# Performance work log

Measured on AMD Instinct MI355X. Metric: run time of the kernel, lower is better.

The kernel has to match this reference:

```python
import jax, jax.numpy as jnp
import numpy as np

B, N, F_DIM = 64, 4096, 64
K_SLOTS, D, N_ITERS = 8, 64, 3
EPS = 1e-8
LN_EPS = 1e-5  # torch LayerNorm default


def layernorm(x, g, b):
    mu = jnp.mean(x, axis=-1, keepdims=True)
    var = jnp.mean(jnp.square(x - mu), axis=-1, keepdims=True)
    return (x - mu) * jax.lax.rsqrt(var + LN_EPS) * g + b


def gru_cell(x, h, w_ih, w_hh, b_ih, b_hh):
    # torch.nn.GRUCell semantics; weights are [3D, D] with gate order r, z, n
    gi = x @ w_ih.T + b_ih
    gh = h @ w_hh.T + b_hh
    i_r, i_z, i_n = jnp.split(gi, 3, axis=-1)
    h_r, h_z, h_n = jnp.split(gh, 3, axis=-1)
    r = jax.nn.sigmoid(i_r + h_r)
    z = jax.nn.sigmoid(i_z + h_z)
    n = jnp.tanh(i_n + r * h_n)
    return (1.0 - z) * n + z * h


def setup_inputs() -> dict:
    key = jax.random.key(0)
    ks = jax.random.split(key, 16)
    f32 = jnp.float32
    s = 0.05  # small init scale for weights
    return {
        "inputs": jax.random.normal(ks[0], (B, N, F_DIM), f32),
        "slots_noise": jax.random.normal(ks[1], (B, K_SLOTS, D), f32),
        "slots_mu": jax.random.normal(ks[2], (1, 1, D), f32) * s,
        "slots_log_sigma": jax.random.normal(ks[3], (1, 1, D), f32) * s,
        "Wq": jax.random.normal(ks[4], (D, D), f32) * s,
        "Wk": jax.random.normal(ks[5], (D, F_DIM), f32) * s,
        "Wv": jax.random.normal(ks[6], (D, F_DIM), f32) * s,
        "gru_w_ih": jax.random.normal(ks[7], (3 * D, D), f32) * s,
        "gru_w_hh": jax.random.normal(ks[8], (3 * D, D), f32) * s,
        "gru_b_ih": jnp.zeros((3 * D,), f32),
        "gru_b_hh": jnp.zeros((3 * D,), f32),
        "mlp_w1": jax.random.normal(ks[9], (2 * D, D), f32) * s,
        "mlp_b1": jnp.zeros((2 * D,), f32),
        "mlp_w2": jax.random.normal(ks[10], (D, 2 * D), f32) * s,
        "mlp_b2": jnp.zeros((D,), f32),
        "ln_in_g": jnp.ones((F_DIM,), f32), "ln_in_b": jnp.zeros((F_DIM,), f32),
        "ln_slots_g": jnp.ones((D,), f32), "ln_slots_b": jnp.zeros((D,), f32),
        "ln_mlp_g": jnp.ones((D,), f32), "ln_mlp_b": jnp.zeros((D,), f32),
    }


def reference(inputs, slots_noise, slots_mu, slots_log_sigma, Wq, Wk, Wv,
              gru_w_ih, gru_w_hh, gru_b_ih, gru_b_hh,
              mlp_w1, mlp_b1, mlp_w2, mlp_b2,
              ln_in_g, ln_in_b, ln_slots_g, ln_slots_b, ln_mlp_g, ln_mlp_b):
    x = layernorm(inputs, ln_in_g, ln_in_b)          # [B, N, F]
    k = jnp.einsum('bnf,df->bnd', x, Wk)             # [B, N, D]
    v = jnp.einsum('bnf,df->bnd', x, Wv)             # [B, N, D]

    slots = slots_mu + jnp.exp(slots_log_sigma) * slots_noise  # [B, K, D]
    scale = D ** -0.5

    for _ in range(N_ITERS):
        slots_prev = slots
        s_n = layernorm(slots, ln_slots_g, ln_slots_b)
        q = jnp.einsum('bkd,ed->bke', s_n, Wq)                  # [B, K, D]
        attn_logits = jnp.einsum('bnd,bkd->bnk', k, q) * scale  # [B, N, K]
        attn = jax.nn.softmax(attn_logits, axis=-1) + EPS       # softmax over slots
        attn = attn / jnp.sum(attn, axis=1, keepdims=True)      # renormalize over N
        updates = jnp.einsum('bnk,bnd->bkd', attn, v)           # [B, K, D]
        slots = gru_cell(updates.reshape(-1, D), slots_prev.reshape(-1, D),
                         gru_w_ih, gru_w_hh, gru_b_ih, gru_b_hh).reshape(B, K_SLOTS, D)
        h = layernorm(slots, ln_mlp_g, ln_mlp_b)
        h = jax.nn.relu(h @ mlp_w1.T + mlp_b1) @ mlp_w2.T + mlp_b2
        slots = slots + h
    return slots
```

## Files before the change

kernel.cpp:

```cpp
#include <hip/hip_runtime.h>
#include <math.h>

#define NN 4096
#define LN_EPS 1e-5f
#define EPS 1e-8f

typedef unsigned short ushortT;
typedef unsigned int uintT;
typedef __attribute__((ext_vector_type(8))) short short8;
typedef __attribute__((ext_vector_type(4))) float f32x4;
typedef __attribute__((ext_vector_type(4))) unsigned short us4;

#define OFF_KT    0L
#define OFF_V     16777216L
#define OFF_QT    33554432L
#define OFF_ACC   33587200L
#define OFF_COL   33619968L
#define OFF_SLOTS 33620480L
#define OFF_WIHT  33653248L
#define OFF_WHHT  33665536L
#define OFF_W1T   33677824L
#define OFF_W2T   33686016L
#define OFF_WQT   33694208L
#define OFF_WKV   33698304L
#define OFF_CNT   33702400L

__device__ __forceinline__ float wredsum(float v) {
#pragma unroll
  for (int off = 32; off > 0; off >>= 1) v += __shfl_xor(v, off);
  return v;
}

__device__ __forceinline__ ushortT f2bf(float f) {
  uintT b = __float_as_uint(f);
  b += 0x7fff + ((b >> 16) & 1);
  return (ushortT)(b >> 16);
}

__global__ __launch_bounds__(256) void k_prep(
    const float* __restrict__ w_ih, const float* __restrict__ w_hh,
    const float* __restrict__ w1, const float* __restrict__ w2,
    const float* __restrict__ Wq,
    const float* __restrict__ Wk, const float* __restrict__ Wv,
    float* __restrict__ wihT, float* __restrict__ whhT,
    float* __restrict__ w1T, float* __restrict__ w2T, float* __restrict__ wqT,
    ushortT* __restrict__ wpack, uintT* __restrict__ cnt)
{
  int idx = blockIdx.x * 256 + threadIdx.x;
  if (idx < 12288) {
    int j = idx >> 6, f = idx & 63;
    wihT[f * 192 + j] = w_ih[idx];
  } else if (idx < 24576) {
    int i = idx - 12288; int j = i >> 6, f = i & 63;
    whhT[f * 192 + j] = w_hh[i];
  } else if (idx < 32768) {
    int i = idx - 24576; int j = i >> 6, f = i & 63;
    w1T[f * 128 + j] = w1[i];
  } else if (idx < 40960) {
    int i = idx - 32768; int d = i >> 7, j = i & 127;
    w2T[j * 64 + d] = w2[i];
  } else if (idx < 45056) {
    int i = idx - 40960; int e = i >> 6, d = i & 63;
    wqT[d * 64 + e] = Wq[i];
  } else if (idx < 53248) {
    int i = idx - 45056;
    int j = i & 7, l = (i >> 3) & 63, t2 = i >> 9;
    int ct = t2 >> 1, kb = t2 & 1;
    int kf = kb * 32 + ((l >> 4) << 3) + j;
    int col = (ct << 4) | (l & 15);
    float val = (col < 64) ? Wk[col * 64 + kf] : Wv[(col - 64) * 64 + kf];
    wpack[i] = f2bf(val);
  } else if (idx < 53312) {
    cnt[idx - 53248] = 0u;
  }
}

__global__ __launch_bounds__(256) void k_ln_init(
    const float* __restrict__ inp, const ushortT* __restrict__ wpack,
    const float* __restrict__ g, const float* __restrict__ bbv,
    ushortT* __restrict__ ktF, ushortT* __restrict__ vF,
    const float* __restrict__ noise, const float* __restrict__ smu,
    const float* __restrict__ slsig, const float* __restrict__ wqT,
    const float* __restrict__ g_sl, const float* __restrict__ b_sl,
    float* __restrict__ slots, ushortT* __restrict__ qF,
    float* __restrict__ acc, float* __restrict__ colsum)
{
  __shared__ __align__(16) ushortT xnF[4096];
  __shared__ __align__(16) ushortT kS[4096];
  const int tid = threadIdx.x;
  const int lane = tid & 63;
  const int wave = tid >> 6;

  if (blockIdx.x >= 4096) {
    const int bi = blockIdx.x - 4096;
    const int row = bi * 4 + wave;
    const int b = row >> 3, ks = row & 7;
    float* S2 = (float*)&xnF[0];

    float s0 = fmaf(expf(slsig[lane]), noise[row * 64 + lane], smu[lane]);
    slots[row * 64 + lane] = s0;
    acc[row * 64 + lane] = 0.f;
    if (lane == 0) colsum[row] = 0.f;

    float mu = wredsum(s0) * (1.f / 64.f);
    float dx = s0 - mu;
    float var = wredsum(dx * dx) * (1.f / 64.f);
    float sn = dx * rsqrtf(var + LN_EPS) * g_sl[lane] + b_sl[lane];
    S2[(wave << 6) + lane] = sn;
    __syncthreads();
    float qe = 0.f;
#pragma unroll 16
    for (int d = 0; d < 64; ++d) qe = fmaf(S2[(wave << 6) + d], wqT[d * 64 + lane], qe);
    const int kb = lane >> 5, lrow = (lane & 31) >> 3, j = lane & 7;
    qF[((((b * 2 + kb) << 6) + (lrow << 4) + ks) << 3) + j] = f2bf(qe * 0.125f);
    qF[((((b * 2 + kb) << 6) + (lrow << 4) + 8 + ks) << 3) + j] = 0;
    return;
  }

  const int l15 = lane & 15, q = lane >> 4;
  const int tile = blockIdx.x;
  const int b = tile >> 6;
  const int c = tile & 63;
  const int n0 = c << 6;
  const float* rowbase = inp + (((long)b * NN + n0) << 6);
  const float4 g4 = *(const float4*)&g[l15 << 2];
  const float4 b4 = *(const float4*)&bbv[l15 << 2];

#pragma unroll
  for (int i = 0; i < 4; ++i) {
    const int row = (wave << 4) + (i << 2) + q;
    float4 x = *(const float4*)&rowbase[(row << 6) + (l15 << 2)];
    float s = x.x + x.y + x.z + x.w;
    s += __shfl_xor(s, 1); s += __shfl_xor(s, 2);
    s += __shfl_xor(s, 4); s += __shfl_xor(s, 8);
    const float mu = s * (1.f / 64.f);
    float4 dx = {x.x - mu, x.y - mu, x.z - mu, x.w - mu};
    float ss = dx.x * dx.x + dx.y * dx.y + dx.z * dx.z + dx.w * dx.w;
    ss += __shfl_xor(ss, 1); ss += __shfl_xor(ss, 2);
    ss += __shfl_xor(ss, 4); ss += __shfl_xor(ss, 8);
    const float rs = rsqrtf(ss * (1.f / 64.f) + LN_EPS);
    us4 p = {f2bf(dx.x * rs * g4.x + b4.x), f2bf(dx.y * rs * g4.y + b4.y),
             f2bf(dx.z * rs * g4.z + b4.z), f2bf(dx.w * rs * g4.w + b4.w)};
    *(us4*)&xnF[((((wave << 1) + (l15 >> 3)) << 6) + (((l15 & 7) >> 1) << 4)
                 + (row & 15)) * 8 + ((l15 & 1) << 2)] = p;
  }

  short8 bfrag[2][2];
#pragma unroll
  for (int nt = 0; nt < 2; ++nt)
#pragma unroll
    for (int kb = 0; kb < 2; ++kb)
      bfrag[nt][kb] = *(const short8*)&wpack[((((2 * wave + nt) << 1) | kb) * 64 + lane) << 3];

  __syncthreads();

  f32x4 acc4[4][2];
#pragma unroll
  for (int mt = 0; mt < 4; ++mt)
#pragma unroll
    for (int nt = 0; nt < 2; ++nt) acc4[mt][nt] = (f32x4){0.f, 0.f, 0.f, 0.f};

#pragma unroll
  for (int mt = 0; mt < 4; ++mt) {
    short8 a0 = *(const short8*)&xnF[((mt * 2 + 0) * 64 + lane) << 3];
    short8 a1 = *(const short8*)&xnF[((mt * 2 + 1) * 64 + lane) << 3];
#pragma unroll
    for (int nt = 0; nt < 2; ++nt) {
      acc4[mt][nt] = __builtin_amdgcn_mfma_f32_16x16x32_bf16(a0, bfrag[nt][0], acc4[mt][nt], 0, 0, 0);
      acc4[mt][nt] = __builtin_amdgcn_mfma_f32_16x16x32_bf16(a1, bfrag[nt][1], acc4[mt][nt], 0, 0, 0);
    }
  }

  if (wave < 2) {
#pragma unroll
    for (int mt = 0; mt < 4; ++mt)
#pragma unroll
      for (int nt = 0; nt < 2; ++nt) {
        const int base = (((mt * 2 + wave) << 6) + ((2 * nt + (l15 >> 3)) << 4) + (q << 2));
#pragma unroll
        for (int r = 0; r < 4; ++r)
          kS[((base + r) << 3) + (l15 & 7)] = f2bf(acc4[mt][nt][r]);
      }
  } else {
    ushortT* vbase = vF + ((long)(b * 64 + c) << 12);
#pragma unroll
    for (int mt = 0; mt < 4; ++mt)
#pragma unroll
      for (int nt = 0; nt < 2; ++nt) {
        const int ntg = 2 * (wave - 2) + nt;
        us4 p = {f2bf(acc4[mt][nt][0]), f2bf(acc4[mt][nt][1]),
                 f2bf(acc4[mt][nt][2]), f2bf(acc4[mt][nt][3])};
        *(us4*)&vbase[(((((ntg << 1) + (mt >> 1)) << 6)
                        + (((mt & 1) * 2 + (q >> 1)) << 4) + l15) << 3)
                      + ((q & 1) << 2)] = p;
      }
  }
  __syncthreads();

  ushortT* kdst = ktF + ((long)(b * 64 + c) << 12);
  short8 v0 = *(const short8*)&kS[tid << 4];
  short8 v1 = *(const short8*)&kS[(tid << 4) + 8];
  *(short8*)&kdst[tid << 4] = v0;
  *(short8*)&kdst[(tid << 4) + 8] = v1;
}

__global__ __launch_bounds__(256) void k_attn(
    const ushortT* __restrict__ ktF, const ushortT* __restrict__ vF,
    ushortT* __restrict__ qF,
    float* __restrict__ acc, float* __restrict__ colsum,
    uintT* __restrict__ cnt, float* __restrict__ slots,
    const float* __restrict__ wihT, const float* __restrict__ whhT,
    const float* __restrict__ w1T, const float* __restrict__ w2T,
    const float* __restrict__ wqT,
    const float* __restrict__ b_ih, const float* __restrict__ b_hh,
    const float* __restrict__ mb1, const float* __restrict__ mb2,
    const float* __restrict__ g_ml, const float* __restrict__ b_ml,
    const float* __restrict__ g_sl, const float* __restrict__ b_sl,
    float* __restrict__ dout)
{
  __shared__ __align__(16) ushortT attnF[4][1024];
  __shared__ float accLds[4][8][64];
  __shared__ float colLds[4][8];
  __shared__ int lastFlag;
  const int tid = threadIdx.x;
  const int lane = tid & 63;
  const int wave = tid >> 6;
  const int l15 = lane & 15, q = lane >> 4;
  const int b = blockIdx.x >> 4;
  const int chunk = ((blockIdx.x & 15) << 2) | wave;

  const ushortT* kbF = ktF + ((long)(b * 64 + chunk) << 12);
  const ushortT* vbF = vF + ((long)(b * 64 + chunk) << 12);

  short8 kA[4][2];
#pragma unroll
  for (int mt = 0; mt < 4; ++mt)
#pragma unroll
    for (int kb = 0; kb < 2; ++kb)
      kA[mt][kb] = *(const short8*)&kbF[((mt * 2 + kb) * 64 + lane) << 3];
  short8 qB[2];
#pragma unroll
  for (int kb = 0; kb < 2; ++kb)
    qB[kb] = *(const short8*)&qF[(((b * 2 + kb) << 6) + lane) << 3];

  f32x4 accL[4];
#pragma unroll
  for (int mt = 0; mt < 4; ++mt) {
    accL[mt] = (f32x4){0.f, 0.f, 0.f, 0.f};
    accL[mt] = __builtin_amdgcn_mfma_f32_16x16x32_bf16(kA[mt][0], qB[0], accL[mt], 0, 0, 0);
    accL[mt] = __builtin_amdgcn_mfma_f32_16x16x32_bf16(kA[mt][1], qB[1], accL[mt], 0, 0, 0);
  }

  short8 vB[4][2];
#pragma unroll
  for (int nt = 0; nt < 4; ++nt)
#pragma unroll
    for (int ks = 0; ks < 2; ++ks)
      vB[nt][ks] = *(const short8*)&vbF[((nt * 2 + ks) * 64 + lane) << 3];

  float csum = 0.f;
#pragma unroll
  for (int mt = 0; mt < 4; ++mt) {
    float av[4];
#pragma unroll
    for (int r = 0; r < 4; ++r) {
      float lv = accL[mt][r];
      float mx = lv;
      mx = fmaxf(mx, __shfl_xor(mx, 1));
      mx = fmaxf(mx, __shfl_xor(mx, 2));
      mx = fmaxf(mx, __shfl_xor(mx, 4));
      float ev = __expf(lv - mx);
      float sv = ev;
      sv += __shfl_xor(sv, 1); sv += __shfl_xor(sv, 2); sv += __shfl_xor(sv, 4);
      float a = ev * (1.f / sv) + EPS;
      av[r] = a;
      csum += a;
    }
    us4 p = {f2bf(av[0]), f2bf(av[1]), f2bf(av[2]), f2bf(av[3])};
    *(us4*)&attnF[wave][((((mt >> 1) << 6) + (((mt & 1) * 2 + (q >> 1)) << 4)
                          + l15) << 3) + ((q & 1) << 2)] = p;
  }
  csum += __shfl_xor(csum, 16);
  csum += __shfl_xor(csum, 32);

  short8 pA0 = *(const short8*)&attnF[wave][(0 * 64 + lane) << 3];
  short8 pA1 = *(const short8*)&attnF[wave][(1 * 64 + lane) << 3];

  f32x4 accP[4];
#pragma unroll
  for (int nt = 0; nt < 4; ++nt) {
    accP[nt] = (f32x4){0.f, 0.f, 0.f, 0.f};
    accP[nt] = __builtin_amdgcn_mfma_f32_16x16x32_bf16(pA0, vB[nt][0], accP[nt], 0, 0, 0);
    accP[nt] = __builtin_amdgcn_mfma_f32_16x16x32_bf16(pA1, vB[nt][1], accP[nt], 0, 0, 0);
  }

  if (q < 2) {
#pragma unroll
    for (int nt = 0; nt < 4; ++nt)
#pragma unroll
      for (int r = 0; r < 4; ++r)
        accLds[wave][q * 4 + r][nt * 16 + l15] = accP[nt][r];
  }
  if (q == 0 && l15 < 8) colLds[wave][l15] = csum;
  __syncthreads();

#pragma unroll
  for (int r = 0; r < 2; ++r) {
    const int o = tid + r * 256;
    const int kk = o >> 6, d = o & 63;
    float s = accLds[0][kk][d] + accLds[1][kk][d] + accLds[2][kk][d] + accLds[3][kk][d];
    atomicAdd(&acc[(b * 8 + kk) * 64 + d], s);
  }
  if (tid < 8) {
    float s = colLds[0][tid] + colLds[1][tid] + colLds[2][tid] + colLds[3][tid];
    atomicAdd(&colsum[b * 8 + tid], s);
  }

  __syncthreads();
  if (tid == 0) lastFlag = (atomicAdd(&cnt[b], 1u) == 15u);
  __syncthreads();
  if (!lastFlag) return;

  const int ks0 = wave, ks1 = wave + 4;
  const int row0 = b * 8 + ks0, row1 = b * 8 + ks1;

  float csv0 = 0.f, csv1 = 0.f;
  if (lane == 0) {
    csv0 = atomicAdd(&colsum[row0], 0.f);
    csv1 = atomicAdd(&colsum[row1], 0.f);
  }
  csv0 = __shfl(csv0, 0); csv1 = __shfl(csv1, 0);
  const float u0 = atomicAdd(&acc[row0 * 64 + lane], 0.f) / csv0;
  const float u1 = atomicAdd(&acc[row1 * 64 + lane], 0.f) / csv1;
  const float h0 = slots[row0 * 64 + lane];
  const float h1 = slots[row1 * 64 + lane];

  float* S = (float*)&attnF[wave][0];
  S[lane] = u0; S[64 + lane] = u1; S[128 + lane] = h0; S[192 + lane] = h1;

  float gir0 = b_ih[lane], giz0 = b_ih[64 + lane], gin0 = b_ih[128 + lane];
  float ghr0 = b_hh[lane], ghz0 = b_hh[64 + lane], ghn0 = b_hh[128 + lane];
  float gir1 = gir0, giz1 = giz0, gin1 = gin0;
  float ghr1 = ghr0, ghz1 = ghz0, ghn1 = ghn0;
#pragma unroll 4
  for (int f = 0; f < 64; ++f) {
    const float wr = wihT[f * 192 + lane], wz = wihT[f * 192 + 64 + lane],
                wn = wihT[f * 192 + 128 + lane];
    const float vr = whhT[f * 192 + lane], vz = whhT[f * 192 + 64 + lane],
                vn = whhT[f * 192 + 128 + lane];
    const float a0 = S[f], a1 = S[64 + f], c0 = S[128 + f], c1 = S[192 + f];
    gir0 = fmaf(a0, wr, gir0); gir1 = fmaf(a1, wr, gir1);
    giz0 = fmaf(a0, wz, giz0); giz1 = fmaf(a1, wz, giz1);
    gin0 = fmaf(a0, wn, gin0); gin1 = fmaf(a1, wn, gin1);
    ghr0 = fmaf(c0, vr, ghr0); ghr1 = fmaf(c1, vr, ghr1);
    ghz0 = fmaf(c0, vz, ghz0); ghz1 = fmaf(c1, vz, ghz1);
    ghn0 = fmaf(c0, vn, ghn0); ghn1 = fmaf(c1, vn, ghn1);
  }
  const float r0 = 1.f / (1.f + expf(-(gir0 + ghr0)));
  const float z0 = 1.f / (1.f + expf(-(giz0 + ghz0)));
  const float n0 = tanhf(fmaf(r0, ghn0, gin0));
  const float hn0 = (1.f - z0) * n0 + z0 * h0;
  const float r1 = 1.f / (1.f + expf(-(gir1 + ghr1)));
  const float z1 = 1.f / (1.f + expf(-(giz1 + ghz1)));
  const float n1 = tanhf(fmaf(r1, ghn1, gin1));
  const float hn1 = (1.f - z1) * n1 + z1 * h1;

  float mu0 = wredsum(hn0) * (1.f / 64.f);
  float dx0 = hn0 - mu0;
  float va0 = wredsum(dx0 * dx0) * (1.f / 64.f);
  const float ln0 = dx0 * rsqrtf(va0 + LN_EPS) * g_ml[lane] + b_ml[lane];
  float mu1 = wredsum(hn1) * (1.f / 64.f);
  float dx1 = hn1 - mu1;
  float va1 = wredsum(dx1 * dx1) * (1.f / 64.f);
  const float ln1 = dx1 * rsqrtf(va1 + LN_EPS) * g_ml[lane] + b_ml[lane];
  S[256 + lane] = ln0; S[320 + lane] = ln1;

  float h1a0 = mb1[lane], h1b0 = mb1[64 + lane];
  float h1a1 = h1a0, h1b1 = h1b0;
#pragma unroll 4
  for (int f = 0; f < 64; ++f) {
    const float wa = w1T[f * 128 + lane], wb = w1T[f * 128 + 64 + lane];
    const float l0 = S[256 + f], l1 = S[320 + f];
    h1a0 = fmaf(l0, wa, h1a0); h1a1 = fmaf(l1, wa, h1a1);
    h1b0 = fmaf(l0, wb, h1b0); h1b1 = fmaf(l1, wb, h1b1);
  }
  h1a0 = fmaxf(h1a0, 0.f); h1b0 = fmaxf(h1b0, 0.f);
  h1a1 = fmaxf(h1a1, 0.f); h1b1 = fmaxf(h1b1, 0.f);
  S[lane] = h1a0; S[64 + lane] = h1b0;
  S[128 + lane] = h1a1; S[192 + lane] = h1b1;

  float o0 = mb2[lane], o1 = mb2[lane];
#pragma unroll 4
  for (int j = 0; j < 128; ++j) {
    const float w2v = w2T[j * 64 + lane];
    o0 = fmaf(S[j], w2v, o0);
    o1 = fmaf(S[128 + j], w2v, o1);
  }
  const float sn0 = hn0 + o0;
  const float sn1 = hn1 + o1;
  slots[row0 * 64 + lane] = sn0;
  slots[row1 * 64 + lane] = sn1;
  if (dout) {
    dout[row0 * 64 + lane] = sn0;
    dout[row1 * 64 + lane] = sn1;
  }

  float m20 = wredsum(sn0) * (1.f / 64.f);
  float d20 = sn0 - m20;
  float v20 = wredsum(d20 * d20) * (1.f / 64.f);
  const float sq0 = d20 * rsqrtf(v20 + LN_EPS) * g_sl[lane] + b_sl[lane];
  float m21 = wredsum(sn1) * (1.f / 64.f);
  float d21 = sn1 - m21;
  float v21 = wredsum(d21 * d21) * (1.f / 64.f);
  const float sq1 = d21 * rsqrtf(v21 + LN_EPS) * g_sl[lane] + b_sl[lane];
  S[256 + lane] = sq0; S[320 + lane] = sq1;
  float qe0 = 0.f, qe1 = 0.f;
#pragma unroll 8
  for (int d = 0; d < 64; ++d) {
    const float wq = wqT[d * 64 + lane];
    qe0 = fmaf(S[256 + d], wq, qe0);
    qe1 = fmaf(S[320 + d], wq, qe1);
  }
  const int kb = lane >> 5, lrow = (lane & 31) >> 3, jj = lane & 7;
  qF[((((b * 2 + kb) << 6) + (lrow << 4) + ks0) << 3) + jj] = f2bf(qe0 * 0.125f);
  qF[((((b * 2 + kb) << 6) + (lrow << 4) + ks1) << 3) + jj] = f2bf(qe1 * 0.125f);

  acc[row0 * 64 + lane] = 0.f;
  acc[row1 * 64 + lane] = 0.f;
  if (lane == 0) { colsum[row0] = 0.f; colsum[row1] = 0.f; }
  if (tid == 0) cnt[b] = 0u;
}

extern "C" void kernel_launch(void* const* d_in, const int* in_sizes, int n_in,
                              void* d_out, int out_size, void* d_ws, size_t ws_size,
                              hipStream_t stream) {
  const float* inp   = (const float*)d_in[0];
  const float* noise = (const float*)d_in[1];
  const float* smu   = (const float*)d_in[2];
  const float* slsig = (const float*)d_in[3];
  const float* Wq    = (const float*)d_in[4];
  const float* Wk    = (const float*)d_in[5];
  const float* Wv    = (const float*)d_in[6];
  const float* w_ih  = (const float*)d_in[7];
  const float* w_hh  = (const float*)d_in[8];
  const float* b_ih  = (const float*)d_in[9];
  const float* b_hh  = (const float*)d_in[10];
  const float* w1    = (const float*)d_in[11];
  const float* b1    = (const float*)d_in[12];
  const float* w2    = (const float*)d_in[13];
  const float* b2    = (const float*)d_in[14];
  const float* g_in  = (const float*)d_in[15];
  const float* bi_in = (const float*)d_in[16];
  const float* g_sl  = (const float*)d_in[17];
  const float* bi_sl = (const float*)d_in[18];
  const float* g_ml  = (const float*)d_in[19];
  const float* bi_ml = (const float*)d_in[20];

  float* ws      = (float*)d_ws;
  ushortT* ktF   = (ushortT*)(ws + OFF_KT);
  ushortT* vF    = (ushortT*)(ws + OFF_V);
  ushortT* qF    = (ushortT*)(ws + OFF_QT);
  float* ac      = ws + OFF_ACC;
  float* cs      = ws + OFF_COL;
  float* sl      = ws + OFF_SLOTS;
  float* wihT    = ws + OFF_WIHT;
  float* whhT    = ws + OFF_WHHT;
  float* w1T     = ws + OFF_W1T;
  float* w2T     = ws + OFF_W2T;
  float* wqT     = ws + OFF_WQT;
  ushortT* wpk   = (ushortT*)(ws + OFF_WKV);
  uintT* cnt     = (uintT*)(ws + OFF_CNT);

  k_prep<<<209, 256, 0, stream>>>(w_ih, w_hh, w1, w2, Wq, Wk, Wv,
                                  wihT, whhT, w1T, w2T, wqT, wpk, cnt);
  k_ln_init<<<4224, 256, 0, stream>>>(inp, wpk, g_in, bi_in, ktF, vF,
                                      noise, smu, slsig, wqT, g_sl, bi_sl,
                                      sl, qF, ac, cs);
  for (int it = 0; it < 3; ++it) {
    k_attn<<<1024, 256, 0, stream>>>(ktF, vF, qF, ac, cs, cnt, sl,
                                     wihT, whhT, w1T, w2T, wqT,
                                     b_ih, b_hh, b1, b2, g_ml, bi_ml, g_sl, bi_sl,
                                     it == 2 ? (float*)d_out : nullptr);
  }
}
```

Before: 259.8 us.

## Fold Wk into query and Wv after aggregation to store only normalized inputs

Instead of materializing K and V (two bf16 tensors) from the layernormed inputs, the kernel stores only the normalized input x once and folds Wk into the query (q·Wk) and applies Wv after the attention-weighted sum of x. This halves the large per-iteration global reads of K/V and removes the K/V MFMA projection from the init kernel. It adds small per-slot matvecs in the attention kernel and an LDS transpose of the x fragments to build the V-side operand. That transpose carries bank-conflict and register costs, and bf16 rounding now happens at different points.

```diff
diff --git a/kernel.cpp b/kernel.cpp
--- a/kernel.cpp
+++ b/kernel.cpp
@@ -11,8 +11,7 @@
 typedef __attribute__((ext_vector_type(4))) float f32x4;
 typedef __attribute__((ext_vector_type(4))) unsigned short us4;
 
-#define OFF_KT    0L
-#define OFF_V     16777216L
+#define OFF_XN    0L
 #define OFF_QT    33554432L
 #define OFF_ACC   33587200L
 #define OFF_COL   33619968L
@@ -22,7 +21,7 @@
 #define OFF_W1T   33677824L
 #define OFF_W2T   33686016L
 #define OFF_WQT   33694208L
-#define OFF_WKV   33698304L
+#define OFF_WVT   33698304L
 #define OFF_CNT   33702400L
 
 __device__ __forceinline__ float wredsum(float v) {
@@ -40,11 +39,10 @@
 __global__ __launch_bounds__(256) void k_prep(
     const float* __restrict__ w_ih, const float* __restrict__ w_hh,
     const float* __restrict__ w1, const float* __restrict__ w2,
-    const float* __restrict__ Wq,
-    const float* __restrict__ Wk, const float* __restrict__ Wv,
+    const float* __restrict__ Wq, const float* __restrict__ Wv,
     float* __restrict__ wihT, float* __restrict__ whhT,
     float* __restrict__ w1T, float* __restrict__ w2T, float* __restrict__ wqT,
-    ushortT* __restrict__ wpack, uintT* __restrict__ cnt)
+    float* __restrict__ wvT, uintT* __restrict__ cnt)
 {
   int idx = blockIdx.x * 256 + threadIdx.x;
   if (idx < 12288) {
@@ -62,31 +60,26 @@
   } else if (idx < 45056) {
     int i = idx - 40960; int e = i >> 6, d = i & 63;
     wqT[d * 64 + e] = Wq[i];
-  } else if (idx < 53248) {
-    int i = idx - 45056;
-    int j = i & 7, l = (i >> 3) & 63, t2 = i >> 9;
-    int ct = t2 >> 1, kb = t2 & 1;
-    int kf = kb * 32 + ((l >> 4) << 3) + j;
-    int col = (ct << 4) | (l & 15);
-    float val = (col < 64) ? Wk[col * 64 + kf] : Wv[(col - 64) * 64 + kf];
-    wpack[i] = f2bf(val);
-  } else if (idx < 53312) {
-    cnt[idx - 53248] = 0u;
+  } else if (idx < 49152) {
+    int i = idx - 45056; int d = i >> 6, f = i & 63;
+    wvT[f * 64 + d] = Wv[i];
+  } else if (idx < 49216) {
+    cnt[idx - 49152] = 0u;
   }
 }
 
 __global__ __launch_bounds__(256) void k_ln_init(
-    const float* __restrict__ inp, const ushortT* __restrict__ wpack,
+    const float* __restrict__ inp,
     const float* __restrict__ g, const float* __restrict__ bbv,
-    ushortT* __restrict__ ktF, ushortT* __restrict__ vF,
+    ushortT* __restrict__ xnG,
     const float* __restrict__ noise, const float* __restrict__ smu,
     const float* __restrict__ slsig, const float* __restrict__ wqT,
+    const float* __restrict__ Wk,
     const float* __restrict__ g_sl, const float* __restrict__ b_sl,
     float* __restrict__ slots, ushortT* __restrict__ qF,
     float* __restrict__ acc, float* __restrict__ colsum)
 {
   __shared__ __align__(16) ushortT xnF[4096];
-  __shared__ __align__(16) ushortT kS[4096];
   const int tid = threadIdx.x;
   const int lane = tid & 63;
   const int wave = tid >> 6;
@@ -95,7 +88,8 @@
     const int bi = blockIdx.x - 4096;
     const int row = bi * 4 + wave;
     const int b = row >> 3, ks = row & 7;
-    float* S2 = (float*)&xnF[0];
+    float* SI = (float*)&xnF[0];
+    float* Sw = SI + (wave << 9);
 
     float s0 = fmaf(expf(slsig[lane]), noise[row * 64 + lane], smu[lane]);
     slots[row * 64 + lane] = s0;
@@ -106,13 +100,16 @@
     float dx = s0 - mu;
     float var = wredsum(dx * dx) * (1.f / 64.f);
     float sn = dx * rsqrtf(var + LN_EPS) * g_sl[lane] + b_sl[lane];
-    S2[(wave << 6) + lane] = sn;
-    __syncthreads();
+    Sw[lane] = sn;
     float qe = 0.f;
 #pragma unroll 16
-    for (int d = 0; d < 64; ++d) qe = fmaf(S2[(wave << 6) + d], wqT[d * 64 + lane], qe);
+    for (int d = 0; d < 64; ++d) qe = fmaf(Sw[d], wqT[d * 64 + lane], qe);
+    Sw[64 + lane] = qe;
+    float qp = 0.f;
+#pragma unroll 16
+    for (int e = 0; e < 64; ++e) qp = fmaf(Sw[64 + e], Wk[e * 64 + lane], qp);
     const int kb = lane >> 5, lrow = (lane & 31) >> 3, j = lane & 7;
-    qF[((((b * 2 + kb) << 6) + (lrow << 4) + ks) << 3) + j] = f2bf(qe * 0.125f);
+    qF[((((b * 2 + kb) << 6) + (lrow << 4) + ks) << 3) + j] = f2bf(qp * 0.125f);
     qF[((((b * 2 + kb) << 6) + (lrow << 4) + 8 + ks) << 3) + j] = 0;
     return;
   }
@@ -144,83 +141,31 @@
     *(us4*)&xnF[((((wave << 1) + (l15 >> 3)) << 6) + (((l15 & 7) >> 1) << 4)
                  + (row & 15)) * 8 + ((l15 & 1) << 2)] = p;
   }
-
-  short8 bfrag[2][2];
-#pragma unroll
-  for (int nt = 0; nt < 2; ++nt)
-#pragma unroll
-    for (int kb = 0; kb < 2; ++kb)
-      bfrag[nt][kb] = *(const short8*)&wpack[((((2 * wave + nt) << 1) | kb) * 64 + lane) << 3];
-
   __syncthreads();
 
-  f32x4 acc4[4][2];
-#pragma unroll
-  for (int mt = 0; mt < 4; ++mt)
-#pragma unroll
-    for (int nt = 0; nt < 2; ++nt) acc4[mt][nt] = (f32x4){0.f, 0.f, 0.f, 0.f};
-
-#pragma unroll
-  for (int mt = 0; mt < 4; ++mt) {
-    short8 a0 = *(const short8*)&xnF[((mt * 2 + 0) * 64 + lane) << 3];
-    short8 a1 = *(const short8*)&xnF[((mt * 2 + 1) * 64 + lane) << 3];
-#pragma unroll
-    for (int nt = 0; nt < 2; ++nt) {
-      acc4[mt][nt] = __builtin_amdgcn_mfma_f32_16x16x32_bf16(a0, bfrag[nt][0], acc4[mt][nt], 0, 0, 0);
-      acc4[mt][nt] = __builtin_amdgcn_mfma_f32_16x16x32_bf16(a1, bfrag[nt][1], acc4[mt][nt], 0, 0, 0);
-    }
-  }
-
-  if (wave < 2) {
-#pragma unroll
-    for (int mt = 0; mt < 4; ++mt)
-#pragma unroll
-      for (int nt = 0; nt < 2; ++nt) {
-        const int base = (((mt * 2 + wave) << 6) + ((2 * nt + (l15 >> 3)) << 4) + (q << 2));
-#pragma unroll
-        for (int r = 0; r < 4; ++r)
-          kS[((base + r) << 3) + (l15 & 7)] = f2bf(acc4[mt][nt][r]);
-      }
-  } else {
-    ushortT* vbase = vF + ((long)(b * 64 + c) << 12);
-#pragma unroll
-    for (int mt = 0; mt < 4; ++mt)
-#pragma unroll
-      for (int nt = 0; nt < 2; ++nt) {
-        const int ntg = 2 * (wave - 2) + nt;
-        us4 p = {f2bf(acc4[mt][nt][0]), f2bf(acc4[mt][nt][1]),
-                 f2bf(acc4[mt][nt][2]), f2bf(acc4[mt][nt][3])};
-        *(us4*)&vbase[(((((ntg << 1) + (mt >> 1)) << 6)
-                        + (((mt & 1) * 2 + (q >> 1)) << 4) + l15) << 3)
-                      + ((q & 1) << 2)] = p;
-      }
-  }
-  __syncthreads();
-
-  ushortT* kdst = ktF + ((long)(b * 64 + c) << 12);
-  short8 v0 = *(const short8*)&kS[tid << 4];
-  short8 v1 = *(const short8*)&kS[(tid << 4) + 8];
-  *(short8*)&kdst[tid << 4] = v0;
-  *(short8*)&kdst[(tid << 4) + 8] = v1;
-}
-
-__global__ __launch_bounds__(256) void k_attn(
-    const ushortT* __restrict__ ktF, const ushortT* __restrict__ vF,
+  ushortT* dst = xnG + ((long)(b * 64 + c) << 12);
+  short8 v0 = *(const short8*)&xnF[tid << 4];
+  short8 v1 = *(const short8*)&xnF[(tid << 4) + 8];
+  *(short8*)&dst[tid << 4] = v0;
+  *(short8*)&dst[(tid << 4) + 8] = v1;
+}
+
+__global__ __launch_bounds__(256, 4) void k_attn(
+    const ushortT* __restrict__ xnG,
     ushortT* __restrict__ qF,
     float* __restrict__ acc, float* __restrict__ colsum,
     uintT* __restrict__ cnt, float* __restrict__ slots,
     const float* __restrict__ wihT, const float* __restrict__ whhT,
     const float* __restrict__ w1T, const float* __restrict__ w2T,
-    const float* __restrict__ wqT,
+    const float* __restrict__ wqT, const float* __restrict__ Wk,
+    const float* __restrict__ wvT,
     const float* __restrict__ b_ih, const float* __restrict__ b_hh,
     const float* __restrict__ mb1, const float* __restrict__ mb2,
     const float* __restrict__ g_ml, const float* __restrict__ b_ml,
     const float* __restrict__ g_sl, const float* __restrict__ b_sl,
     float* __restrict__ dout)
 {
-  __shared__ __align__(16) ushortT attnF[4][1024];
-  __shared__ float accLds[4][8][64];
-  __shared__ float colLds[4][8];
+  __shared__ __align__(16) ushortT XW[4][4096];
   __shared__ int lastFlag;
   const int tid = threadIdx.x;
   const int lane = tid & 63;
@@ -229,8 +174,9 @@
   const int b = blockIdx.x >> 4;
   const int chunk = ((blockIdx.x & 15) << 2) | wave;
 
-  const ushortT* kbF = ktF + ((long)(b * 64 + chunk) << 12);
-  const ushortT* vbF = vF + ((long)(b * 64 + chunk) << 12);
+  ushortT* xT = &XW[wave][0];
+
+  const ushortT* kbF = xnG + ((long)(b * 64 + chunk) << 12);
 
   short8 kA[4][2];
 #pragma unroll
@@ -251,13 +197,33 @@
     accL[mt] = __builtin_amdgcn_mfma_f32_16x16x32_bf16(kA[mt][1], qB[1], accL[mt], 0, 0, 0);
   }
 
+  {
+    const int h = ((lane >> 5) << 2) | (((lane & 15) >> 3) << 1) | ((lane >> 4) & 1);
+    const int jp = lane & 7;
+    const int lpA = (((lane >> 4) & 1) << 3) + (((lane & 15) >> 3) << 4);
+#pragma unroll
+    for (int mt = 0; mt < 4; ++mt)
+#pragma unroll
+      for (int kb = 0; kb < 2; ++kb) {
+        const int fb = (kb * 4 + ((lane >> 5) << 1) + (mt >> 1)) << 9;
+        const int lm = lpA + ((mt & 1) << 5);
+        const ushortT* src = (const ushortT*)&kA[mt][kb];
+#pragma unroll
+        for (int j = 0; j < 8; ++j)
+          xT[fb + (((lm + j) ^ h) << 3) + jp] = src[j];
+      }
+  }
   short8 vB[4][2];
 #pragma unroll
   for (int nt = 0; nt < 4; ++nt)
 #pragma unroll
-    for (int ks = 0; ks < 2; ++ks)
-      vB[nt][ks] = *(const short8*)&vbF[((nt * 2 + ks) * 64 + lane) << 3];
-
+    for (int ks = 0; ks < 2; ++ks) {
+      const int frag = nt * 2 + ks;
+      const int hr = ((nt & 1) << 2) | (((lane >> 4) & 1) << 1) | ((lane >> 3) & 1);
+      vB[nt][ks] = *(const short8*)&xT[(frag << 9) + ((lane ^ hr) << 3)];
+    }
+
+  ushortT* attnF = &XW[wave][0];
   float csum = 0.f;
 #pragma unroll
   for (int mt = 0; mt < 4; ++mt) {
@@ -277,14 +243,14 @@
       csum += a;
     }
     us4 p = {f2bf(av[0]), f2bf(av[1]), f2bf(av[2]), f2bf(av[3])};
-    *(us4*)&attnF[wave][((((mt >> 1) << 6) + (((mt & 1) * 2 + (q >> 1)) << 4)
-                          + l15) << 3) + ((q & 1) << 2)] = p;
+    *(us4*)&attnF[((((mt >> 1) << 6) + (((mt & 1) * 2 + (q >> 1)) << 4)
+                    + l15) << 3) + ((q & 1) << 2)] = p;
   }
   csum += __shfl_xor(csum, 16);
   csum += __shfl_xor(csum, 32);
 
-  short8 pA0 = *(const short8*)&attnF[wave][(0 * 64 + lane) << 3];
-  short8 pA1 = *(const short8*)&attnF[wave][(1 * 64 + lane) << 3];
+  short8 pA0 = *(const short8*)&attnF[(0 * 64 + lane) << 3];
+  short8 pA1 = *(const short8*)&attnF[(1 * 64 + lane) << 3];
 
   f32x4 accP[4];
 #pragma unroll
@@ -294,25 +260,31 @@
     accP[nt] = __builtin_amdgcn_mfma_f32_16x16x32_bf16(pA1, vB[nt][1], accP[nt], 0, 0, 0);
   }
 
+  float* accLw = (float*)&XW[wave][1024];
+  float* colLw = (float*)&XW[wave][2048];
   if (q < 2) {
 #pragma unroll
     for (int nt = 0; nt < 4; ++nt)
 #pragma unroll
       for (int r = 0; r < 4; ++r)
-        accLds[wave][q * 4 + r][nt * 16 + l15] = accP[nt][r];
-  }
-  if (q == 0 && l15 < 8) colLds[wave][l15] = csum;
+        accLw[(q * 4 + r) * 64 + nt * 16 + l15] = accP[nt][r];
+  }
+  if (q == 0 && l15 < 8) colLw[l15] = csum;
   __syncthreads();
 
 #pragma unroll
   for (int r = 0; r < 2; ++r) {
     const int o = tid + r * 256;
     const int kk = o >> 6, d = o & 63;
-    float s = accLds[0][kk][d] + accLds[1][kk][d] + accLds[2][kk][d] + accLds[3][kk][d];
+    float s = *((float*)&XW[0][1024] + kk * 64 + d)
+            + *((float*)&XW[1][1024] + kk * 64 + d)
+            + *((float*)&XW[2][1024] + kk * 64 + d)
+            + *((float*)&XW[3][1024] + kk * 64 + d);
     atomicAdd(&acc[(b * 8 + kk) * 64 + d], s);
   }
   if (tid < 8) {
-    float s = colLds[0][tid] + colLds[1][tid] + colLds[2][tid] + colLds[3][tid];
+    float s = *((float*)&XW[0][2048] + tid) + *((float*)&XW[1][2048] + tid)
+            + *((float*)&XW[2][2048] + tid) + *((float*)&XW[3][2048] + tid);
     atomicAdd(&colsum[b * 8 + tid], s);
   }
 
@@ -330,12 +302,22 @@
     csv1 = atomicAdd(&colsum[row1], 0.f);
   }
   csv0 = __shfl(csv0, 0); csv1 = __shfl(csv1, 0);
-  const float u0 = atomicAdd(&acc[row0 * 64 + lane], 0.f) / csv0;
-  const float u1 = atomicAdd(&acc[row1 * 64 + lane], 0.f) / csv1;
+  const float t0 = atomicAdd(&acc[row0 * 64 + lane], 0.f) / csv0;
+  const float t1 = atomicAdd(&acc[row1 * 64 + lane], 0.f) / csv1;
   const float h0 = slots[row0 * 64 + lane];
   const float h1 = slots[row1 * 64 + lane];
 
-  float* S = (float*)&attnF[wave][0];
+  float* S = (float*)&XW[wave][0];
+
+  S[256 + lane] = t0; S[320 + lane] = t1;
+  float u0 = 0.f, u1 = 0.f;
+#pragma unroll 4
+  for (int f = 0; f < 64; ++f) {
+    const float wv = wvT[f * 64 + lane];
+    u0 = fmaf(S[256 + f], wv, u0);
+    u1 = fmaf(S[320 + f], wv, u1);
+  }
+
   S[lane] = u0; S[64 + lane] = u1; S[128 + lane] = h0; S[192 + lane] = h1;
 
   float gir0 = b_ih[lane], giz0 = b_ih[64 + lane], gin0 = b_ih[128 + lane];
@@ -421,9 +403,17 @@
     qe0 = fmaf(S[256 + d], wq, qe0);
     qe1 = fmaf(S[320 + d], wq, qe1);
   }
+  S[384 + lane] = qe0; S[448 + lane] = qe1;
+  float qp0 = 0.f, qp1 = 0.f;
+#pragma unroll 8
+  for (int e = 0; e < 64; ++e) {
+    const float wk = Wk[e * 64 + lane];
+    qp0 = fmaf(S[384 + e], wk, qp0);
+    qp1 = fmaf(S[448 + e], wk, qp1);
+  }
   const int kb = lane >> 5, lrow = (lane & 31) >> 3, jj = lane & 7;
-  qF[((((b * 2 + kb) << 6) + (lrow << 4) + ks0) << 3) + jj] = f2bf(qe0 * 0.125f);
-  qF[((((b * 2 + kb) << 6) + (lrow << 4) + ks1) << 3) + jj] = f2bf(qe1 * 0.125f);
+  qF[((((b * 2 + kb) << 6) + (lrow << 4) + ks0) << 3) + jj] = f2bf(qp0 * 0.125f);
+  qF[((((b * 2 + kb) << 6) + (lrow << 4) + ks1) << 3) + jj] = f2bf(qp1 * 0.125f);
 
   acc[row0 * 64 + lane] = 0.f;
   acc[row1 * 64 + lane] = 0.f;
@@ -457,8 +447,7 @@
   const float* bi_ml = (const float*)d_in[20];
 
   float* ws      = (float*)d_ws;
-  ushortT* ktF   = (ushortT*)(ws + OFF_KT);
-  ushortT* vF    = (ushortT*)(ws + OFF_V);
+  ushortT* xnG   = (ushortT*)(ws + OFF_XN);
   ushortT* qF    = (ushortT*)(ws + OFF_QT);
   float* ac      = ws + OFF_ACC;
   float* cs      = ws + OFF_COL;
@@ -468,17 +457,17 @@
   float* w1T     = ws + OFF_W1T;
   float* w2T     = ws + OFF_W2T;
   float* wqT     = ws + OFF_WQT;
-  ushortT* wpk   = (ushortT*)(ws + OFF_WKV);
+  float* wvT     = ws + OFF_WVT;
   uintT* cnt     = (uintT*)(ws + OFF_CNT);
 
-  k_prep<<<209, 256, 0, stream>>>(w_ih, w_hh, w1, w2, Wq, Wk, Wv,
-                                  wihT, whhT, w1T, w2T, wqT, wpk, cnt);
-  k_ln_init<<<4224, 256, 0, stream>>>(inp, wpk, g_in, bi_in, ktF, vF,
-                                      noise, smu, slsig, wqT, g_sl, bi_sl,
+  k_prep<<<193, 256, 0, stream>>>(w_ih, w_hh, w1, w2, Wq, Wv,
+                                  wihT, whhT, w1T, w2T, wqT, wvT, cnt);
+  k_ln_init<<<4224, 256, 0, stream>>>(inp, g_in, bi_in, xnG,
+                                      noise, smu, slsig, wqT, Wk, g_sl, bi_sl,
                                       sl, qF, ac, cs);
   for (int it = 0; it < 3; ++it) {
-    k_attn<<<1024, 256, 0, stream>>>(ktF, vF, qF, ac, cs, cnt, sl,
-                                     wihT, whhT, w1T, w2T, wqT,
+    k_attn<<<1024, 256, 0, stream>>>(xnG, qF, ac, cs, cnt, sl,
+                                     wihT, whhT, w1T, w2T, wqT, Wk, wvT,
                                      b_ih, b_hh, b1, b2, g_ml, bi_ml, g_sl, bi_sl,
                                      it == 2 ? (float*)d_out : nullptr);
   }
```

New measurement: 271.9 us. 4.6% more time.
